# Kernel optimization log

Measured on AMD Instinct MI355X. Metric: run time of the kernel, lower is better.

## Reference

```python
import jax, jax.numpy as jnp
import numpy as np

K = 32        # number of negative samples
MARGIN = 1.0  # ranking margin
N_NODES = 8192
D_FEAT = 128
N_ANCHOR = 512
CHUNK = 128   # anchor chunk for cdist to bound the [chunk,N,d] intermediate


def l1_cdist(X, Y):
    # X: [A, d], Y: [N, d] -> [A, N]; chunk over A so the abs-diff tensor
    # is [CHUNK, N, d] (~0.5GB here) instead of [A, N, d].
    A, d = X.shape
    def f(xc):  # xc: [CHUNK, d]
        return jnp.sum(jnp.abs(xc[:, None, :] - Y[None, :, :]), axis=-1)
    out = jax.lax.map(f, X.reshape(-1, CHUNK, d))  # [A/CHUNK, CHUNK, N]
    return out.reshape(A, Y.shape[0])


def l1_rowdist(a, b):
    # a, b: [..., d] -> [...]: per-row L1 distance
    return jnp.sum(jnp.abs(a - b), axis=-1)


def setup_inputs() -> dict:
    key = jax.random.key(0)
    k1, k2, k3, k4 = jax.random.split(key, 4)
    out1 = jax.random.normal(k1, (N_NODES, D_FEAT), dtype=jnp.float32)
    out2 = jax.random.normal(k2, (N_NODES, D_FEAT), dtype=jnp.float32)
    anchor1 = jax.random.randint(k3, (N_ANCHOR,), 0, N_NODES, dtype=jnp.int64 if jax.config.jax_enable_x64 else jnp.int32)
    anchor2 = jax.random.randint(k4, (N_ANCHOR,), 0, N_NODES, dtype=jnp.int64 if jax.config.jax_enable_x64 else jnp.int32)
    return {"out1": out1, "out2": out2, "anchor1": anchor1, "anchor2": anchor2}


def reference(out1, out2, anchor1, anchor2):
    a1 = out1[anchor1]  # [A, d]
    a2 = out2[anchor2]  # [A, d]

    # Negative sampling: k NEAREST nodes in the other graph (argsort ascending,
    # take first k). Indices only -> no gradient path (matches numpy detach).
    _, neg1 = jax.lax.top_k(-l1_cdist(a1, out2), K)  # [A, K] into out2
    _, neg2 = jax.lax.top_k(-l1_cdist(a2, out1), K)  # [A, K] into out1

    neg_emb1 = out2[neg1]  # [A, K, d]
    neg_emb2 = out1[neg2]  # [A, K, d]

    D = l1_rowdist(a1, a2) + MARGIN          # [A]
    B1 = -l1_rowdist(a1[:, None, :], neg_emb1)  # [A, K]
    B2 = -l1_rowdist(a2[:, None, :], neg_emb2)  # [A, K]

    L1 = jnp.sum(jax.nn.relu(D[:, None] + B1))
    L2 = jnp.sum(jax.nn.relu(D[:, None] + B2))
    return (L1 + L2) / (anchor1.shape[0] * K)
```

## Files before the change

kernel.cpp:

```cpp
#include <hip/hip_runtime.h>


#define NN 8192
#define DF 128
#define NA 512
#define KK 32
#define CCAP 256


__device__ __forceinline__ float wave_reduce_f(float x) {
#pragma unroll
  for (int off = 32; off > 0; off >>= 1) x += __shfl_down(x, off);
  return x;
}

__device__ __forceinline__ int wave_reduce_i(int x) {
#pragma unroll
  for (int off = 32; off > 0; off >>= 1) x += __shfl_down(x, off);
  return x;
}

__device__ __forceinline__ unsigned umin2(unsigned a, unsigned b) {
  return a < b ? a : b;
}

__device__ __forceinline__ unsigned sad16(unsigned a, unsigned b,
                                          unsigned acc) {
#if __has_builtin(__builtin_amdgcn_sad_u16)
  return __builtin_amdgcn_sad_u16(a, b, acc);
#else
  const unsigned al = a & 0xFFFFu, bl = b & 0xFFFFu;
  const unsigned ah = a >> 16, bh = b >> 16;
  acc += (al > bl) ? (al - bl) : (bl - al);
  acc += (ah > bh) ? (ah - bh) : (bh - ah);
  return acc;
#endif
}

__device__ __forceinline__ unsigned q2(float x, float y) {
  const unsigned lo = (unsigned)fmaf(x, 4096.0f, 32768.5f);
  const unsigned hi = (unsigned)fmaf(y, 4096.0f, 32768.5f);
  return lo | (hi << 16);
}

__device__ __forceinline__ uint4 quant8(float4 a, float4 b) {
  uint4 r;
  r.x = q2(a.x, a.y);
  r.y = q2(a.z, a.w);
  r.z = q2(b.x, b.y);
  r.w = q2(b.z, b.w);
  return r;
}


__global__ __launch_bounds__(256, 3) void dist_kernel(
    const float* __restrict__ out1, const float* __restrict__ out2,
    const int* __restrict__ anchor1, const int* __restrict__ anchor2,
    float* __restrict__ dist) {
  const int tid = threadIdx.x;
  const int nb = blockIdx.x;
  const int ab = blockIdx.y;
  const int dir = blockIdx.z;
  const float* nodes = dir ? out1 : out2;
  const float* asrc = dir ? out2 : out1;
  const int* aidx = dir ? anchor2 : anchor1;
  const int n0 = nb * 128;
  const int a0 = ab * 64;

  __shared__ union {
    struct {
      unsigned nds[128][20];
      unsigned ads[64][20];
    } t;
    float stage[32][136];
  } sm;
  __shared__ int aind[64];

  if (tid < 64) aind[tid] = aidx[a0 + tid];

  unsigned acc[8][4];
#pragma unroll
  for (int i = 0; i < 8; ++i)
#pragma unroll
    for (int j = 0; j < 4; ++j) acc[i][j] = 0u;

  const int tn = tid & 15;
  const int ta = tid >> 4;

#pragma unroll 1
  for (int cch = 0; cch < 4; ++cch) {
    const int d0 = cch * 32;
    __syncthreads();
#pragma unroll
    for (int r = 0; r < 2; ++r) {
      const int f = tid + 256 * r;
      const int row = f >> 2;
      const int q = f & 3;
      const float* src = nodes + (size_t)(n0 + row) * DF + d0 + q * 8;
      const float4 v0 = *(const float4*)(src);
      const float4 v1 = *(const float4*)(src + 4);
      *(uint4*)&sm.t.nds[row][q * 4] = quant8(v0, v1);
    }
    {
      const int row = tid >> 2;
      const int q = tid & 3;
      const float* src = asrc + (size_t)aind[row] * DF + d0 + q * 8;
      const float4 v0 = *(const float4*)(src);
      const float4 v1 = *(const float4*)(src + 4);
      *(uint4*)&sm.t.ads[row][q * 4] = quant8(v0, v1);
    }
    __syncthreads();
#pragma unroll 1
    for (int d4 = 0; d4 < 8; ++d4) {
      uint2 nv[8], av[4];
#pragma unroll
      for (int i = 0; i < 8; ++i)
        nv[i] = *(const uint2*)&sm.t.nds[tn + 16 * i][d4 * 2];
#pragma unroll
      for (int j = 0; j < 4; ++j)
        av[j] = *(const uint2*)&sm.t.ads[ta + 16 * j][d4 * 2];
#pragma unroll
      for (int i = 0; i < 8; ++i)
#pragma unroll
        for (int j = 0; j < 4; ++j) {
          const unsigned s = sad16(nv[i].x, av[j].x, acc[i][j]);
          acc[i][j] = sad16(nv[i].y, av[j].y, s);
        }
    }
  }

  const float inv = 1.0f / 4096.0f;
  const size_t rowbase = (size_t)(dir * NA + a0) * NN + n0;
#pragma unroll
  for (int half = 0; half < 2; ++half) {
    __syncthreads();
#pragma unroll
    for (int j = 0; j < 2; ++j) {
      const int jj = half * 2 + j;
#pragma unroll
      for (int i = 0; i < 8; ++i)
        sm.stage[ta + 16 * j][tn + 16 * i] = (float)acc[i][jj] * inv;
    }
    __syncthreads();
#pragma unroll
    for (int s = 0; s < 4; ++s) {
      const int f = tid + 256 * s;
      const int row = f >> 5;
      const int c4 = f & 31;
      const float4 v = *(const float4*)&sm.stage[row][c4 * 4];
      *(float4*)(dist + rowbase + (size_t)(half * 32 + row) * NN + c4 * 4) = v;
    }
  }
}


__global__ __launch_bounds__(256) void select_kernel(
    const float* __restrict__ dist, const float* __restrict__ out1,
    const float* __restrict__ out2, const int* __restrict__ anchor1,
    const int* __restrict__ anchor2, float* __restrict__ out) {
  const int tid = threadIdx.x;
  const int lane = tid & 63, w = tid >> 6;
  const int row = blockIdx.x;
  const int a = row & (NA - 1);

  __shared__ unsigned mins[256];
  __shared__ unsigned cand[CCAP];
  __shared__ int cnt;
  __shared__ unsigned Tsh;
  __shared__ float dred[2];

  const uint4* drow = (const uint4*)(dist + (size_t)row * NN);

  {
    float p = 0.f;
    if (tid < DF) {
      const int r1 = anchor1[a];
      const int r2 = anchor2[a];
      p = fabsf(out1[(size_t)r1 * DF + tid] - out2[(size_t)r2 * DF + tid]);
    }
    p = wave_reduce_f(p);
    if (tid < DF && lane == 0) dred[w] = p;
  }
  if (tid == 0) cnt = 0;

  unsigned m0 = 0xFFFFFFFFu, m1 = 0xFFFFFFFFu, m2 = 0xFFFFFFFFu,
           m3 = 0xFFFFFFFFu;
#pragma unroll
  for (int g = 0; g < 8; ++g) {
    const uint4 t = drow[tid + 256 * g];
    m0 = umin2(m0, t.x);
    m1 = umin2(m1, t.y);
    m2 = umin2(m2, t.z);
    m3 = umin2(m3, t.w);
  }
  mins[tid] = umin2(umin2(m0, m1), umin2(m2, m3));
  __syncthreads();

  if (w == 0) {
    const unsigned pm =
        umin2(umin2(mins[lane], mins[lane + 64]),
              umin2(mins[lane + 128], mins[lane + 192]));
    unsigned T = 0;
#pragma unroll 1
    for (int b = 30; b >= 0; --b) {
      const unsigned mid = T | (1u << b);
      if ((int)__popcll(__ballot(pm < mid)) < KK) T = mid;
    }
    if (lane == 0) Tsh = T;
  }
  __syncthreads();
  const unsigned T = Tsh;

#pragma unroll
  for (int g = 0; g < 8; ++g) {
    const uint4 t = drow[tid + 256 * g];
    if (t.x <= T) { int q = atomicAdd(&cnt, 1); if (q < CCAP) cand[q] = t.x; }
    if (t.y <= T) { int q = atomicAdd(&cnt, 1); if (q < CCAP) cand[q] = t.y; }
    if (t.z <= T) { int q = atomicAdd(&cnt, 1); if (q < CCAP) cand[q] = t.z; }
    if (t.w <= T) { int q = atomicAdd(&cnt, 1); if (q < CCAP) cand[q] = t.w; }
  }
  __syncthreads();
  const int C = cnt;
  const float Dv = dred[0] + dred[1] + 1.0f;

  if (w != 0) return;

  if (C <= CCAP) {
    unsigned v[4];
#pragma unroll
    for (int k = 0; k < 4; ++k)
      v[k] = (lane + 64 * k < C) ? cand[lane + 64 * k] : 0xFFFFFFFFu;

    unsigned P = 0;
#pragma unroll 1
    for (int b = 30; b >= 0; --b) {
      const unsigned mid = P | (1u << b);
      int c = 0;
#pragma unroll
      for (int k = 0; k < 4; ++k) c += (int)__popcll(__ballot(v[k] < mid));
      if (c < KK) P = mid;
    }

    float s = 0.f;
    int c = 0;
#pragma unroll
    for (int k = 0; k < 4; ++k) {
      c += (int)__popcll(__ballot(v[k] < P));
      if (v[k] < P) {
        const float t = Dv - __uint_as_float(v[k]);
        s += (t > 0.f) ? t : 0.f;
      }
    }
    s = wave_reduce_f(s);
    if (lane == 0) {
      float tt = Dv - __uint_as_float(P);
      if (tt < 0.f) tt = 0.f;
      atomicAdd(out, (s + (float)(KK - c) * tt) * (1.0f / (float)(NA * KK)));
    }
  } else {
    unsigned P = 0;
#pragma unroll 1
    for (int b = 30; b >= 0; --b) {
      const unsigned mid = P | (1u << b);
      int c = 0;
#pragma unroll 1
      for (int g = 0; g < 32; ++g) {
        const uint4 t = drow[lane + 64 * g];
        c += (int)__popcll(__ballot(t.x < mid));
        c += (int)__popcll(__ballot(t.y < mid));
        c += (int)__popcll(__ballot(t.z < mid));
        c += (int)__popcll(__ballot(t.w < mid));
      }
      if (c < KK) P = mid;
    }
    float s = 0.f;
    int c = 0;
#pragma unroll 1
    for (int g = 0; g < 32; ++g) {
      const uint4 t = drow[lane + 64 * g];
      const unsigned vv[4] = {t.x, t.y, t.z, t.w};
#pragma unroll
      for (int k = 0; k < 4; ++k) {
        c += (int)__popcll(__ballot(vv[k] < P));
        if (vv[k] < P) {
          const float tt = Dv - __uint_as_float(vv[k]);
          s += (tt > 0.f) ? tt : 0.f;
        }
      }
    }
    s = wave_reduce_f(s);
    if (lane == 0) {
      float tt = Dv - __uint_as_float(P);
      if (tt < 0.f) tt = 0.f;
      atomicAdd(out, (s + (float)(KK - c) * tt) * (1.0f / (float)(NA * KK)));
    }
  }
}


__device__ __forceinline__ float compute_D_block(
    const float* __restrict__ out1, const float* __restrict__ out2,
    const int* __restrict__ anchor1, const int* __restrict__ anchor2, int a) {
  __shared__ float dred[4];
  const int tid = threadIdx.x;
  float p = 0.f;
  if (tid < DF) {
    const int r1 = anchor1[a];
    const int r2 = anchor2[a];
    p = fabsf(out1[(size_t)r1 * DF + tid] - out2[(size_t)r2 * DF + tid]);
  }
  p = wave_reduce_f(p);
  const int lane = tid & 63, wid = tid >> 6;
  if (lane == 0) dred[wid] = p;
  __syncthreads();
  return dred[0] + dred[1] + dred[2] + dred[3] + 1.0f;
}

__global__ __launch_bounds__(256) void fused_kernel(
    const float* __restrict__ out1, const float* __restrict__ out2,
    const int* __restrict__ anchor1, const int* __restrict__ anchor2,
    float* __restrict__ out) {
  const int tid = threadIdx.x;
  const int row = blockIdx.x;
  const int dir = row >> 9;
  const int a = row & (NA - 1);
  const float* nodes = dir ? out1 : out2;
  const float* asrc = dir ? out2 : out1;
  const int* aidx = dir ? anchor2 : anchor1;

  __shared__ float ars[DF];
  __shared__ int redi[4];
  __shared__ float redf[4];
  if (tid < DF / 4) {
    const int arow = aidx[a];
    *(float4*)&ars[tid * 4] =
        *(const float4*)(asrc + (size_t)arow * DF + tid * 4);
  }
  __syncthreads();

  unsigned u[32];
  for (int i = 0; i < 32; ++i) {
    const int n = tid + 256 * i;
    const float4* nrow = (const float4*)(nodes + (size_t)n * DF);
    float dsum = 0.f;
    for (int d4 = 0; d4 < DF / 4; ++d4) {
      const float4 t = nrow[d4];
      const float4 av = *(const float4*)&ars[d4 * 4];
      dsum += fabsf(t.x - av.x) + fabsf(t.y - av.y) + fabsf(t.z - av.z) +
              fabsf(t.w - av.w);
    }
    u[i] = __float_as_uint(dsum);
  }
  __syncthreads();

  const float Dv = compute_D_block(out1, out2, anchor1, anchor2, a);
  const int lane = tid & 63, wid = tid >> 6;

  unsigned P = 0;
#pragma unroll 1
  for (int b = 30; b >= 0; --b) {
    const unsigned mid = P | (1u << b);
    int c = 0;
#pragma unroll
    for (int i = 0; i < 32; ++i) c += (u[i] < mid) ? 1 : 0;
    c = wave_reduce_i(c);
    __syncthreads();
    if (lane == 0) redi[wid] = c;
    __syncthreads();
    const int tot = redi[0] + redi[1] + redi[2] + redi[3];
    if (tot < KK) P = mid;
  }

  float s = 0.f;
  int c = 0;
#pragma unroll
  for (int i = 0; i < 32; ++i) {
    if (u[i] < P) {
      const float t = Dv - __uint_as_float(u[i]);
      s += (t > 0.f) ? t : 0.f;
      c += 1;
    }
  }
  s = wave_reduce_f(s);
  c = wave_reduce_i(c);
  __syncthreads();
  if (lane == 0) {
    redf[wid] = s;
    redi[wid] = c;
  }
  __syncthreads();
  if (tid == 0) {
    float stot = redf[0] + redf[1] + redf[2] + redf[3];
    const int ctot = redi[0] + redi[1] + redi[2] + redi[3];
    float tt = Dv - __uint_as_float(P);
    if (tt < 0.f) tt = 0.f;
    stot += (float)(KK - ctot) * tt;
    atomicAdd(out, stot * (1.0f / (float)(NA * KK)));
  }
}


extern "C" void kernel_launch(void* const* d_in, const int* in_sizes, int n_in,
                              void* d_out, int out_size, void* d_ws,
                              size_t ws_size, hipStream_t stream) {
  const float* out1 = (const float*)d_in[0];
  const float* out2 = (const float*)d_in[1];
  const int* anchor1 = (const int*)d_in[2];
  const int* anchor2 = (const int*)d_in[3];
  float* out = (float*)d_out;

  (void)hipMemsetAsync(d_out, 0, sizeof(float), stream);

  const size_t need = (size_t)2 * NA * NN * sizeof(float);
  if (ws_size >= need) {
    float* dist = (float*)d_ws;
    dim3 g1(NN / 128, NA / 64, 2);
    dist_kernel<<<g1, 256, 0, stream>>>(out1, out2, anchor1, anchor2, dist);
    select_kernel<<<2 * NA, 256, 0, stream>>>(dist, out1, out2, anchor1,
                                              anchor2, out);
  } else {
    fused_kernel<<<2 * NA, 256, 0, stream>>>(out1, out2, anchor1, anchor2, out);
  }
}
```

Baseline: 121.0 us.

## Store L1 distance matrix as 16-bit quantized values and keep rows in registers

The distance workspace is now written as 16-bit fixed-point values (the accumulated distance rounded down by 7 bits, giving a 1/32 step) instead of fp32, halving the write and read traffic between the distance and selection kernels. The selection kernel loads each row once into registers, runs 16-bit radix threshold searches, and rewrites the overflow path to use all four waves with block reductions instead of rescanning global memory. The coarser quantization can change which neighbours count as the top-K when distances tie, which slightly perturbs the loss.

```diff
diff --git a/kernel.cpp b/kernel.cpp
--- a/kernel.cpp
+++ b/kernel.cpp
@@ -22,6 +22,10 @@
 
 __device__ __forceinline__ unsigned umin2(unsigned a, unsigned b) {
   return a < b ? a : b;
+}
+
+__device__ __forceinline__ unsigned minpair(unsigned w_) {
+  return umin2(w_ & 0xFFFFu, w_ >> 16);
 }
 
 __device__ __forceinline__ unsigned sad16(unsigned a, unsigned b,
@@ -56,7 +60,7 @@
 __global__ __launch_bounds__(256, 3) void dist_kernel(
     const float* __restrict__ out1, const float* __restrict__ out2,
     const int* __restrict__ anchor1, const int* __restrict__ anchor2,
-    float* __restrict__ dist) {
+    unsigned short* __restrict__ dist16) {
   const int tid = threadIdx.x;
   const int nb = blockIdx.x;
   const int ab = blockIdx.y;
@@ -72,7 +76,7 @@
       unsigned nds[128][20];
       unsigned ads[64][20];
     } t;
-    float stage[32][136];
+    unsigned short stage16[32][136];
   } sm;
   __shared__ int aind[64];
 
@@ -129,7 +133,6 @@
     }
   }
 
-  const float inv = 1.0f / 4096.0f;
   const size_t rowbase = (size_t)(dir * NA + a0) * NN + n0;
 #pragma unroll
   for (int half = 0; half < 2; ++half) {
@@ -138,24 +141,26 @@
     for (int j = 0; j < 2; ++j) {
       const int jj = half * 2 + j;
 #pragma unroll
-      for (int i = 0; i < 8; ++i)
-        sm.stage[ta + 16 * j][tn + 16 * i] = (float)acc[i][jj] * inv;
-    }
-    __syncthreads();
-#pragma unroll
-    for (int s = 0; s < 4; ++s) {
+      for (int i = 0; i < 8; ++i) {
+        const unsigned q16 = umin2((acc[i][jj] + 64u) >> 7, 65535u);
+        sm.stage16[ta + 16 * j][tn + 16 * i] = (unsigned short)q16;
+      }
+    }
+    __syncthreads();
+#pragma unroll
+    for (int s = 0; s < 2; ++s) {
       const int f = tid + 256 * s;
-      const int row = f >> 5;
-      const int c4 = f & 31;
-      const float4 v = *(const float4*)&sm.stage[row][c4 * 4];
-      *(float4*)(dist + rowbase + (size_t)(half * 32 + row) * NN + c4 * 4) = v;
+      const int r = f >> 4;
+      const int c8 = f & 15;
+      const uint4 v = *(const uint4*)&sm.stage16[r][c8 * 8];
+      *(uint4*)(dist16 + rowbase + (size_t)(half * 32 + r) * NN + c8 * 8) = v;
     }
   }
 }
 
 
 __global__ __launch_bounds__(256) void select_kernel(
-    const float* __restrict__ dist, const float* __restrict__ out1,
+    const unsigned short* __restrict__ dist16, const float* __restrict__ out1,
     const float* __restrict__ out2, const int* __restrict__ anchor1,
     const int* __restrict__ anchor2, float* __restrict__ out) {
   const int tid = threadIdx.x;
@@ -168,8 +173,12 @@
   __shared__ int cnt;
   __shared__ unsigned Tsh;
   __shared__ float dred[2];
-
-  const uint4* drow = (const uint4*)(dist + (size_t)row * NN);
+  __shared__ int wcnt[4];
+  __shared__ float fred[4];
+  __shared__ int cred[4];
+
+  const uint4* drow = (const uint4*)(dist16 + (size_t)row * NN);
+  const float inv = 1.0f / 32.0f;
 
   {
     float p = 0.f;
@@ -183,17 +192,19 @@
   }
   if (tid == 0) cnt = 0;
 
-  unsigned m0 = 0xFFFFFFFFu, m1 = 0xFFFFFFFFu, m2 = 0xFFFFFFFFu,
-           m3 = 0xFFFFFFFFu;
-#pragma unroll
-  for (int g = 0; g < 8; ++g) {
-    const uint4 t = drow[tid + 256 * g];
-    m0 = umin2(m0, t.x);
-    m1 = umin2(m1, t.y);
-    m2 = umin2(m2, t.z);
-    m3 = umin2(m3, t.w);
-  }
-  mins[tid] = umin2(umin2(m0, m1), umin2(m2, m3));
+  uint4 v4[4];
+#pragma unroll
+  for (int g = 0; g < 4; ++g) v4[g] = drow[tid + 256 * g];
+
+  unsigned m = 0xFFFFFFFFu;
+#pragma unroll
+  for (int g = 0; g < 4; ++g) {
+    m = umin2(m, minpair(v4[g].x));
+    m = umin2(m, minpair(v4[g].y));
+    m = umin2(m, minpair(v4[g].z));
+    m = umin2(m, minpair(v4[g].w));
+  }
+  mins[tid] = m;
   __syncthreads();
 
   if (w == 0) {
@@ -202,7 +213,7 @@
               umin2(mins[lane + 128], mins[lane + 192]));
     unsigned T = 0;
 #pragma unroll 1
-    for (int b = 30; b >= 0; --b) {
+    for (int b = 15; b >= 0; --b) {
       const unsigned mid = T | (1u << b);
       if ((int)__popcll(__ballot(pm < mid)) < KK) T = mid;
     }
@@ -212,20 +223,21 @@
   const unsigned T = Tsh;
 
 #pragma unroll
-  for (int g = 0; g < 8; ++g) {
-    const uint4 t = drow[tid + 256 * g];
-    if (t.x <= T) { int q = atomicAdd(&cnt, 1); if (q < CCAP) cand[q] = t.x; }
-    if (t.y <= T) { int q = atomicAdd(&cnt, 1); if (q < CCAP) cand[q] = t.y; }
-    if (t.z <= T) { int q = atomicAdd(&cnt, 1); if (q < CCAP) cand[q] = t.z; }
-    if (t.w <= T) { int q = atomicAdd(&cnt, 1); if (q < CCAP) cand[q] = t.w; }
+  for (int g = 0; g < 4; ++g) {
+    const unsigned ww[4] = {v4[g].x, v4[g].y, v4[g].z, v4[g].w};
+#pragma unroll
+    for (int k = 0; k < 4; ++k) {
+      const unsigned lo = ww[k] & 0xFFFFu, hi = ww[k] >> 16;
+      if (lo <= T) { int q = atomicAdd(&cnt, 1); if (q < CCAP) cand[q] = lo; }
+      if (hi <= T) { int q = atomicAdd(&cnt, 1); if (q < CCAP) cand[q] = hi; }
+    }
   }
   __syncthreads();
   const int C = cnt;
   const float Dv = dred[0] + dred[1] + 1.0f;
 
-  if (w != 0) return;
-
   if (C <= CCAP) {
+    if (w != 0) return;
     unsigned v[4];
 #pragma unroll
     for (int k = 0; k < 4; ++k)
@@ -233,7 +245,7 @@
 
     unsigned P = 0;
 #pragma unroll 1
-    for (int b = 30; b >= 0; --b) {
+    for (int b = 15; b >= 0; --b) {
       const unsigned mid = P | (1u << b);
       int c = 0;
 #pragma unroll
@@ -247,52 +259,71 @@
     for (int k = 0; k < 4; ++k) {
       c += (int)__popcll(__ballot(v[k] < P));
       if (v[k] < P) {
-        const float t = Dv - __uint_as_float(v[k]);
+        const float t = Dv - (float)v[k] * inv;
         s += (t > 0.f) ? t : 0.f;
       }
     }
     s = wave_reduce_f(s);
     if (lane == 0) {
-      float tt = Dv - __uint_as_float(P);
+      float tt = Dv - (float)P * inv;
       if (tt < 0.f) tt = 0.f;
       atomicAdd(out, (s + (float)(KK - c) * tt) * (1.0f / (float)(NA * KK)));
     }
   } else {
     unsigned P = 0;
 #pragma unroll 1
-    for (int b = 30; b >= 0; --b) {
+    for (int b = 15; b >= 0; --b) {
       const unsigned mid = P | (1u << b);
       int c = 0;
-#pragma unroll 1
-      for (int g = 0; g < 32; ++g) {
-        const uint4 t = drow[lane + 64 * g];
-        c += (int)__popcll(__ballot(t.x < mid));
-        c += (int)__popcll(__ballot(t.y < mid));
-        c += (int)__popcll(__ballot(t.z < mid));
-        c += (int)__popcll(__ballot(t.w < mid));
+#pragma unroll
+      for (int g = 0; g < 4; ++g) {
+        const unsigned ww[4] = {v4[g].x, v4[g].y, v4[g].z, v4[g].w};
+#pragma unroll
+        for (int k = 0; k < 4; ++k) {
+          c += (int)__popcll(__ballot((ww[k] & 0xFFFFu) < mid));
+          c += (int)__popcll(__ballot((ww[k] >> 16) < mid));
+        }
       }
-      if (c < KK) P = mid;
+      if (lane == 0) wcnt[w] = c;
+      __syncthreads();
+      const int tot = wcnt[0] + wcnt[1] + wcnt[2] + wcnt[3];
+      __syncthreads();
+      if (tot < KK) P = mid;
     }
     float s = 0.f;
     int c = 0;
-#pragma unroll 1
-    for (int g = 0; g < 32; ++g) {
-      const uint4 t = drow[lane + 64 * g];
-      const unsigned vv[4] = {t.x, t.y, t.z, t.w};
+#pragma unroll
+    for (int g = 0; g < 4; ++g) {
+      const unsigned ww[4] = {v4[g].x, v4[g].y, v4[g].z, v4[g].w};
 #pragma unroll
       for (int k = 0; k < 4; ++k) {
-        c += (int)__popcll(__ballot(vv[k] < P));
-        if (vv[k] < P) {
-          const float tt = Dv - __uint_as_float(vv[k]);
-          s += (tt > 0.f) ? tt : 0.f;
+        const unsigned lo = ww[k] & 0xFFFFu, hi = ww[k] >> 16;
+        if (lo < P) {
+          const float t = Dv - (float)lo * inv;
+          s += (t > 0.f) ? t : 0.f;
+          c += 1;
+        }
+        if (hi < P) {
+          const float t = Dv - (float)hi * inv;
+          s += (t > 0.f) ? t : 0.f;
+          c += 1;
         }
       }
     }
     s = wave_reduce_f(s);
+    c = wave_reduce_i(c);
     if (lane == 0) {
-      float tt = Dv - __uint_as_float(P);
+      fred[w] = s;
+      cred[w] = c;
+    }
+    __syncthreads();
+    if (tid == 0) {
+      const float stot = fred[0] + fred[1] + fred[2] + fred[3];
+      const int ctot = cred[0] + cred[1] + cred[2] + cred[3];
+      float tt = Dv - (float)P * inv;
       if (tt < 0.f) tt = 0.f;
-      atomicAdd(out, (s + (float)(KK - c) * tt) * (1.0f / (float)(NA * KK)));
+      atomicAdd(out,
+                (stot + (float)(KK - ctot) * tt) * (1.0f / (float)(NA * KK)));
     }
   }
 }
@@ -411,12 +442,12 @@
 
   (void)hipMemsetAsync(d_out, 0, sizeof(float), stream);
 
-  const size_t need = (size_t)2 * NA * NN * sizeof(float);
+  const size_t need = (size_t)2 * NA * NN * sizeof(unsigned short);
   if (ws_size >= need) {
-    float* dist = (float*)d_ws;
+    unsigned short* dist16 = (unsigned short*)d_ws;
     dim3 g1(NN / 128, NA / 64, 2);
-    dist_kernel<<<g1, 256, 0, stream>>>(out1, out2, anchor1, anchor2, dist);
-    select_kernel<<<2 * NA, 256, 0, stream>>>(dist, out1, out2, anchor1,
+    dist_kernel<<<g1, 256, 0, stream>>>(out1, out2, anchor1, anchor2, dist16);
+    select_kernel<<<2 * NA, 256, 0, stream>>>(dist16, out1, out2, anchor1,
                                               anchor2, out);
   } else {
     fused_kernel<<<2 * NA, 256, 0, stream>>>(out1, out2, anchor1, anchor2, out);
```

After: 115.1 us. 1.05x faster.
